# Performance work log

Hardware: AMD Instinct MI355X
Metric: run time of the kernel (lower is better)

## Reference

```python
import jax, jax.numpy as jnp
import numpy as np


def _step(state):
    # state: [B, H, W] in {0.0, 1.0}
    p = jnp.pad(state, ((0, 0), (1, 1), (1, 1)))
    neighbors = (p[:, :-2, :-2] + p[:, :-2, 1:-1] + p[:, :-2, 2:]
                 + p[:, 1:-1, :-2] + p[:, 1:-1, 2:]
                 + p[:, 2:, :-2] + p[:, 2:, 1:-1] + p[:, 2:, 2:])
    alive = state > 0.5
    survives = alive & ((neighbors == 2.0) | (neighbors == 3.0))
    born = (~alive) & (neighbors == 3.0)
    return jnp.where(survives | born, jnp.ones_like(state), jnp.zeros_like(state))


def setup_inputs() -> dict:
    key = jax.random.key(0)
    k1, k2 = jax.random.split(key)
    B, H, W = 32, 1024, 1024
    # Binary occupancy grids in {0.0, 1.0} as the rule expects
    initial_state = (jax.random.uniform(k1, (B, H, W)) > 0.5).astype(jnp.float32)
    target = (jax.random.uniform(k2, (B, H, W)) > 0.5).astype(jnp.float32)
    return {"initial_state": initial_state, "target": target, "generations": 8}


def reference(initial_state, target, generations):
    state = initial_state
    for _ in range(generations):  # small fixed unroll, strict sequential dependency
        state = _step(state)
    error = state - target
    loss = jnp.mean(error * error)
    live_cells = state.sum()
    max_abs_error = jnp.abs(error).max()
    return loss, state, target, live_cells, max_abs_error
```

## Files before the change

### kernel.cpp

```cpp
#include <hip/hip_runtime.h>
#include <cstdint>

typedef unsigned long long u64;

#define BATCH   32
#define H       1024
#define W       1024
#define WPR     16
#define GENS    8
#define HALO    8
#define NTOT    33554432ULL

#define PK_THREADS 256
#define PK_WAVES   4
#define PK_ROWS_PER_BLOCK 32
#define PK_GRID    ((BATCH * H) / PK_ROWS_PER_BLOCK)

__device__ __forceinline__ u64 shflxor64(u64 v, int m) {
    return (u64)__shfl_xor((long long)v, m, 64);
}

__global__ __launch_bounds__(PK_THREADS)
void gol_pack(const float* __restrict__ in_state, u64* __restrict__ packed)
{
    const int tid  = threadIdx.x;
    const int wave = tid >> 6;
    const int lane = tid & 63;
    const int sub  = lane & 15;
    const int wsub = lane >> 4;

    const int row0 = blockIdx.x * PK_ROWS_PER_BLOCK;
    for (int rr = wave; rr < PK_ROWS_PER_BLOCK; rr += PK_WAVES) {
        int row = row0 + rr;
        const float4* rowp4 = (const float4*)(in_state + (size_t)row * W);
        u64* prow = packed + (size_t)row * WPR;
        #pragma unroll
        for (int g = 0; g < 4; ++g) {
            float4 f = rowp4[g * 64 + lane];
            u64 nib = (u64)((f.x > 0.5f) | ((f.y > 0.5f) << 1) |
                            ((f.z > 0.5f) << 2) | ((f.w > 0.5f) << 3));
            u64 v = nib << (sub * 4);
            v |= shflxor64(v, 1);
            v |= shflxor64(v, 2);
            v |= shflxor64(v, 4);
            v |= shflxor64(v, 8);
            if (sub == 0)
                prow[g * 4 + wsub] = v;
        }
    }
}

#define TR      32
#define BR      (TR + 2*HALO)
#define BRP     (BR + 2)
#define WP      (WPR + 2)
#define THREADS 256
#define NWAVES  (THREADS/64)
#define GRID    (BATCH * (H / TR))

__global__ __launch_bounds__(THREADS)
void gol_life(const u64* __restrict__ packed,
              const float* __restrict__ target,
              float* __restrict__ out,
              u64* __restrict__ counters)
{
    __shared__ u64 buf[2][BRP][WP];
    __shared__ unsigned int wsum[NWAVES];

    const int tile = blockIdx.x;
    const int tpb  = H / TR;
    const int b    = tile / tpb;
    const int r0   = (tile - b * tpb) * TR;

    const int tid  = threadIdx.x;
    const int wave = tid >> 6;
    const int lane = tid & 63;

    for (int i = tid; i < 2 * BRP * WP; i += THREADS)
        ((u64*)buf)[i] = 0ULL;
    __syncthreads();

    const u64* packedb = packed + (size_t)b * H * WPR;
    #pragma unroll
    for (int k = 0; k < (BR * WPR) / THREADS; ++k) {
        int idx = tid + k * THREADS;
        int br = idx >> 4;
        int c  = idx & 15;
        int gr = r0 - HALO + br;
        if (gr >= 0 && gr < H)
            buf[0][br + 1][c + 1] = packedb[(size_t)gr * WPR + c];
    }
    __syncthreads();

    int cur = 0;
    for (int step = 0; step < GENS; ++step) {
        #pragma unroll
        for (int k = 0; k < (BR * WPR) / THREADS; ++k) {
            int idx = tid + k * THREADS;
            int br = idx >> 4;
            int c  = (idx & 15) + 1;
            int r  = br + 1;
            int gr = r0 - HALO + br;

            u64 uL = buf[cur][r-1][c-1], uC = buf[cur][r-1][c], uR = buf[cur][r-1][c+1];
            u64 mL = buf[cur][r  ][c-1], mC = buf[cur][r  ][c], mR = buf[cur][r  ][c+1];
            u64 dL = buf[cur][r+1][c-1], dC = buf[cur][r+1][c], dR = buf[cur][r+1][c+1];

            u64 uw = (uC << 1) | (uL >> 63), ue = (uC >> 1) | (uR << 63);
            u64 mw = (mC << 1) | (mL >> 63), me = (mC >> 1) | (mR << 63);
            u64 dw = (dC << 1) | (dL >> 63), de = (dC >> 1) | (dR << 63);
            u64 o0 = uw ^ uC ^ ue, t0 = (uw & uC) | (ue & (uw ^ uC));
            u64 o1 = mw ^ mC ^ me, t1 = (mw & mC) | (me & (mw ^ mC));
            u64 o2 = dw ^ dC ^ de, t2 = (dw & dC) | (de & (dw ^ dC));

            u64 oa = o0 ^ o1 ^ o2;
            u64 oc = (o0 & o1) | (o2 & (o0 ^ o1));
            u64 ts = t0 ^ t1 ^ t2;
            u64 tc = (t0 & t1) | (t2 & (t0 ^ t1));
            u64 b1 = oc ^ ts;
            u64 cc = oc & ts;
            u64 b2 = cc ^ tc;
            u64 b3 = cc & tc;
            u64 eq3 = oa & b1 & ~(b2 | b3);
            u64 eq4 = (~oa) & (~b1) & b2 & (~b3);
            u64 nxtw = eq3 | (mC & eq4);

            buf[cur ^ 1][r][c] = (gr >= 0 && gr < H) ? nxtw : 0ULL;
        }
        __syncthreads();
        cur ^= 1;
    }

    float* o_state = out + 1;
    float* o_tgt   = out + 1 + NTOT;
    const size_t boff = (size_t)b * H * W;

    unsigned int mism = 0, live = 0;
    for (int lr = wave; lr < TR; lr += NWAVES) {
        int br = HALO + lr;
        int gr = r0 + lr;
        size_t rowbase = boff + (size_t)gr * W;
        const u64* wrow = &buf[cur][br + 1][1];
        const float* trow = target + rowbase;
        float* osrow = o_state + rowbase;
        float* otrow = o_tgt + rowbase;
        #pragma unroll
        for (int g = 0; g < 4; ++g) {
            int k = g * 64 + lane;
            if (k < 255) {
                int bitbase = 4 * k + 3;
                int w0 = bitbase >> 6;
                int sh = bitbase & 63;
                u64 lo = wrow[w0];
                u64 hi = wrow[w0 + 1];
                unsigned bits = (unsigned)(((lo >> sh) | (hi << (64 - sh))) & 0xFULL);
                float4 t = *(const float4*)(trow + bitbase);
                unsigned tb = (unsigned)((t.x > 0.5f) | ((t.y > 0.5f) << 1) |
                                         ((t.z > 0.5f) << 2) | ((t.w > 0.5f) << 3));
                mism += (unsigned)__popc(bits ^ tb);
                live += (unsigned)__popc(bits);
                float4 sv;
                sv.x = (float)(bits & 1u);
                sv.y = (float)((bits >> 1) & 1u);
                sv.z = (float)((bits >> 2) & 1u);
                sv.w = (float)((bits >> 3) & 1u);
                *(float4*)(osrow + bitbase) = sv;
                *(float4*)(otrow + bitbase) = t;
            } else {
                u64 wfirst = wrow[0];
                u64 wlast  = wrow[15];
                unsigned hb   = (unsigned)(wfirst & 7ULL);
                unsigned tbit = (unsigned)(wlast >> 63);
                float t0 = trow[0], t1 = trow[1], t2 = trow[2], t3 = trow[1023];
                unsigned htb = (unsigned)((t0 > 0.5f) | ((t1 > 0.5f) << 1) | ((t2 > 0.5f) << 2));
                unsigned ttb = (unsigned)(t3 > 0.5f);
                mism += (unsigned)__popc(hb ^ htb) + (tbit ^ ttb);
                live += (unsigned)__popc(hb) + tbit;
                osrow[0] = (float)(hb & 1u);
                osrow[1] = (float)((hb >> 1) & 1u);
                osrow[2] = (float)((hb >> 2) & 1u);
                osrow[1023] = (float)tbit;
                otrow[0] = t0; otrow[1] = t1; otrow[2] = t2; otrow[1023] = t3;
            }
        }
    }

    unsigned int comb = (mism << 16) | live;
    #pragma unroll
    for (int m = 1; m < 64; m <<= 1)
        comb += (unsigned int)__shfl_xor((int)comb, m, 64);
    if (lane == 0) wsum[wave] = comb;
    __syncthreads();

    if (tid == 0) {
        unsigned int bm = 0, bl = 0;
        #pragma unroll
        for (int i = 0; i < NWAVES; ++i) {
            bm += wsum[i] >> 16;
            bl += wsum[i] & 0xFFFFu;
        }
        atomicAdd(counters, ((u64)bm << 32) | (u64)bl);
    }
}

__global__ void gol_finalize(const u64* __restrict__ counters,
                             float* __restrict__ out)
{
    u64 c = *counters;
    unsigned int mism = (unsigned int)(c >> 32);
    unsigned int live = (unsigned int)(c & 0xFFFFFFFFULL);
    out[0]            = (float)((double)mism / (double)NTOT);
    out[1 + 2*NTOT]   = (float)live;
    out[2 + 2*NTOT]   = (mism > 0) ? 1.0f : 0.0f;
}

extern "C" void kernel_launch(void* const* d_in, const int* in_sizes, int n_in,
                              void* d_out, int out_size, void* d_ws, size_t ws_size,
                              hipStream_t stream) {
    (void)in_sizes; (void)n_in; (void)out_size; (void)ws_size;
    const float* in_state = (const float*)d_in[0];
    const float* target   = (const float*)d_in[1];
    float* out = (float*)d_out;

    u64* counters = (u64*)d_ws;
    u64* packed   = (u64*)((char*)d_ws + 256);

    hipMemsetAsync(d_ws, 0, sizeof(u64), stream);

    gol_pack<<<dim3(PK_GRID), dim3(PK_THREADS), 0, stream>>>(in_state, packed);
    gol_life<<<dim3(GRID), dim3(THREADS), 0, stream>>>(packed, target, out, counters);
    gol_finalize<<<1, 1, 0, stream>>>(counters, out);
}
```

Measured before the change: 468.5 us.

## Split life compute from unpack/output and use nontemporal loads and stores

Moves the float unpack, target copy and reduction out of the Life stencil kernel into a separate unpack kernel that reads the packed result from a workspace buffer. The stencil kernel stays small and compute-bound, and the unpack kernel runs as a streaming pass with one block per 32 rows. Nontemporal loads and stores are added for the large float streams to reduce cache pollution. This costs an extra kernel launch and an extra round trip of the packed state through global memory.

```diff
diff --git a/kernel.cpp b/kernel.cpp
--- a/kernel.cpp
+++ b/kernel.cpp
@@ -2,6 +2,7 @@
 #include <cstdint>
 
 typedef unsigned long long u64;
+typedef float f4v __attribute__((ext_vector_type(4)));
 
 #define BATCH   32
 #define H       1024
@@ -10,11 +11,12 @@
 #define GENS    8
 #define HALO    8
 #define NTOT    33554432ULL
+#define NROWS   (BATCH * H)
 
 #define PK_THREADS 256
 #define PK_WAVES   4
 #define PK_ROWS_PER_BLOCK 32
-#define PK_GRID    ((BATCH * H) / PK_ROWS_PER_BLOCK)
+#define PK_GRID    (NROWS / PK_ROWS_PER_BLOCK)
 
 __device__ __forceinline__ u64 shflxor64(u64 v, int m) {
     return (u64)__shfl_xor((long long)v, m, 64);
@@ -32,11 +34,11 @@
     const int row0 = blockIdx.x * PK_ROWS_PER_BLOCK;
     for (int rr = wave; rr < PK_ROWS_PER_BLOCK; rr += PK_WAVES) {
         int row = row0 + rr;
-        const float4* rowp4 = (const float4*)(in_state + (size_t)row * W);
+        const f4v* rowp4 = (const f4v*)(in_state + (size_t)row * W);
         u64* prow = packed + (size_t)row * WPR;
         #pragma unroll
         for (int g = 0; g < 4; ++g) {
-            float4 f = rowp4[g * 64 + lane];
+            f4v f = __builtin_nontemporal_load(&rowp4[g * 64 + lane]);
             u64 nib = (u64)((f.x > 0.5f) | ((f.y > 0.5f) << 1) |
                             ((f.z > 0.5f) << 2) | ((f.w > 0.5f) << 3));
             u64 v = nib << (sub * 4);
@@ -54,18 +56,13 @@
 #define BR      (TR + 2*HALO)
 #define BRP     (BR + 2)
 #define WP      (WPR + 2)
-#define THREADS 256
-#define NWAVES  (THREADS/64)
-#define GRID    (BATCH * (H / TR))
-
-__global__ __launch_bounds__(THREADS)
-void gol_life(const u64* __restrict__ packed,
-              const float* __restrict__ target,
-              float* __restrict__ out,
-              u64* __restrict__ counters)
+#define LF_THREADS 256
+#define LF_GRID (BATCH * (H / TR))
+
+__global__ __launch_bounds__(LF_THREADS)
+void gol_life(const u64* __restrict__ packedI, u64* __restrict__ packedO)
 {
     __shared__ u64 buf[2][BRP][WP];
-    __shared__ unsigned int wsum[NWAVES];
 
     const int tile = blockIdx.x;
     const int tpb  = H / TR;
@@ -73,17 +70,15 @@
     const int r0   = (tile - b * tpb) * TR;
 
     const int tid  = threadIdx.x;
-    const int wave = tid >> 6;
-    const int lane = tid & 63;
-
-    for (int i = tid; i < 2 * BRP * WP; i += THREADS)
+
+    for (int i = tid; i < 2 * BRP * WP; i += LF_THREADS)
         ((u64*)buf)[i] = 0ULL;
     __syncthreads();
 
-    const u64* packedb = packed + (size_t)b * H * WPR;
-    #pragma unroll
-    for (int k = 0; k < (BR * WPR) / THREADS; ++k) {
-        int idx = tid + k * THREADS;
+    const u64* packedb = packedI + (size_t)b * H * WPR;
+    #pragma unroll
+    for (int k = 0; k < (BR * WPR) / LF_THREADS; ++k) {
+        int idx = tid + k * LF_THREADS;
         int br = idx >> 4;
         int c  = idx & 15;
         int gr = r0 - HALO + br;
@@ -95,8 +90,8 @@
     int cur = 0;
     for (int step = 0; step < GENS; ++step) {
         #pragma unroll
-        for (int k = 0; k < (BR * WPR) / THREADS; ++k) {
-            int idx = tid + k * THREADS;
+        for (int k = 0; k < (BR * WPR) / LF_THREADS; ++k) {
+            int idx = tid + k * LF_THREADS;
             int br = idx >> 4;
             int c  = (idx & 15) + 1;
             int r  = br + 1;
@@ -131,16 +126,50 @@
         cur ^= 1;
     }
 
+    const size_t Rbase = (size_t)b * H + r0;
+    #pragma unroll
+    for (int k = 0; k < (TR * WPR) / LF_THREADS; ++k) {
+        int idx = tid + k * LF_THREADS;
+        int lr = idx >> 4;
+        int c  = idx & 15;
+        packedO[(Rbase + lr) * WPR + c] = buf[cur][HALO + lr + 1][c + 1];
+    }
+}
+
+#define UP_THREADS 256
+#define UP_WAVES   4
+#define RPB        32
+#define UP_GRID    (NROWS / RPB)
+
+__global__ __launch_bounds__(UP_THREADS)
+void gol_unpack(const u64* __restrict__ packedS,
+                const float* __restrict__ target,
+                float* __restrict__ out,
+                u64* __restrict__ counters)
+{
+    __shared__ u64 rows[RPB][WPR + 1];
+    __shared__ unsigned int wsum[UP_WAVES];
+
+    const int tid  = threadIdx.x;
+    const int wave = tid >> 6;
+    const int lane = tid & 63;
+    const int R0   = blockIdx.x * RPB;
+
+    #pragma unroll
+    for (int k = 0; k < (RPB * WPR) / UP_THREADS; ++k) {
+        int idx = tid + k * UP_THREADS;
+        rows[idx >> 4][idx & 15] = packedS[(size_t)R0 * WPR + idx];
+    }
+    if (tid < RPB) rows[tid][WPR] = 0ULL;
+    __syncthreads();
+
     float* o_state = out + 1;
     float* o_tgt   = out + 1 + NTOT;
-    const size_t boff = (size_t)b * H * W;
 
     unsigned int mism = 0, live = 0;
-    for (int lr = wave; lr < TR; lr += NWAVES) {
-        int br = HALO + lr;
-        int gr = r0 + lr;
-        size_t rowbase = boff + (size_t)gr * W;
-        const u64* wrow = &buf[cur][br + 1][1];
+    for (int lr = wave; lr < RPB; lr += UP_WAVES) {
+        size_t rowbase = (size_t)(R0 + lr) * W;
+        const u64* wrow = rows[lr];
         const float* trow = target + rowbase;
         float* osrow = o_state + rowbase;
         float* otrow = o_tgt + rowbase;
@@ -154,18 +183,18 @@
                 u64 lo = wrow[w0];
                 u64 hi = wrow[w0 + 1];
                 unsigned bits = (unsigned)(((lo >> sh) | (hi << (64 - sh))) & 0xFULL);
-                float4 t = *(const float4*)(trow + bitbase);
+                f4v t = __builtin_nontemporal_load((const f4v*)(trow + bitbase));
                 unsigned tb = (unsigned)((t.x > 0.5f) | ((t.y > 0.5f) << 1) |
                                          ((t.z > 0.5f) << 2) | ((t.w > 0.5f) << 3));
                 mism += (unsigned)__popc(bits ^ tb);
                 live += (unsigned)__popc(bits);
-                float4 sv;
+                f4v sv;
                 sv.x = (float)(bits & 1u);
                 sv.y = (float)((bits >> 1) & 1u);
                 sv.z = (float)((bits >> 2) & 1u);
                 sv.w = (float)((bits >> 3) & 1u);
-                *(float4*)(osrow + bitbase) = sv;
-                *(float4*)(otrow + bitbase) = t;
+                __builtin_nontemporal_store(sv, (f4v*)(osrow + bitbase));
+                __builtin_nontemporal_store(t,  (f4v*)(otrow + bitbase));
             } else {
                 u64 wfirst = wrow[0];
                 u64 wlast  = wrow[15];
@@ -176,11 +205,14 @@
                 unsigned ttb = (unsigned)(t3 > 0.5f);
                 mism += (unsigned)__popc(hb ^ htb) + (tbit ^ ttb);
                 live += (unsigned)__popc(hb) + tbit;
-                osrow[0] = (float)(hb & 1u);
-                osrow[1] = (float)((hb >> 1) & 1u);
-                osrow[2] = (float)((hb >> 2) & 1u);
-                osrow[1023] = (float)tbit;
-                otrow[0] = t0; otrow[1] = t1; otrow[2] = t2; otrow[1023] = t3;
+                __builtin_nontemporal_store((float)(hb & 1u),        osrow);
+                __builtin_nontemporal_store((float)((hb >> 1) & 1u), osrow + 1);
+                __builtin_nontemporal_store((float)((hb >> 2) & 1u), osrow + 2);
+                __builtin_nontemporal_store((float)tbit,             osrow + 1023);
+                __builtin_nontemporal_store(t0, otrow);
+                __builtin_nontemporal_store(t1, otrow + 1);
+                __builtin_nontemporal_store(t2, otrow + 2);
+                __builtin_nontemporal_store(t3, otrow + 1023);
             }
         }
     }
@@ -195,7 +227,7 @@
     if (tid == 0) {
         unsigned int bm = 0, bl = 0;
         #pragma unroll
-        for (int i = 0; i < NWAVES; ++i) {
+        for (int i = 0; i < UP_WAVES; ++i) {
             bm += wsum[i] >> 16;
             bl += wsum[i] & 0xFFFFu;
         }
@@ -223,11 +255,13 @@
     float* out = (float*)d_out;
 
     u64* counters = (u64*)d_ws;
-    u64* packed   = (u64*)((char*)d_ws + 256);
+    u64* packedI  = (u64*)((char*)d_ws + 4096);
+    u64* packedO  = (u64*)((char*)d_ws + 4096 + (4u << 20));
 
     hipMemsetAsync(d_ws, 0, sizeof(u64), stream);
 
-    gol_pack<<<dim3(PK_GRID), dim3(PK_THREADS), 0, stream>>>(in_state, packed);
-    gol_life<<<dim3(GRID), dim3(THREADS), 0, stream>>>(packed, target, out, counters);
+    gol_pack  <<<dim3(PK_GRID), dim3(PK_THREADS), 0, stream>>>(in_state, packedI);
+    gol_life  <<<dim3(LF_GRID), dim3(LF_THREADS), 0, stream>>>(packedI, packedO);
+    gol_unpack<<<dim3(UP_GRID), dim3(UP_THREADS), 0, stream>>>(packedO, target, out, counters);
     gol_finalize<<<1, 1, 0, stream>>>(counters, out);
 }
```

Result: slower. 488.7 us (+4.3%).
